# Optimization experiments

Measured on AMD Instinct MI355X. Metric: run time of the kernel, lower is better.

The kernel has to match this reference:

```python
import jax, jax.numpy as jnp
import numpy as np

NEIGHBOR_NUM = 4
POOLING_RATE = 4


def setup_inputs() -> dict:
    key = jax.random.key(0)
    k1, k2, k3 = jax.random.split(key, 3)
    B, N, C = 4, 8192, 256
    vertices = jax.random.normal(k1, (B, N, 3), dtype=jnp.float32)
    feature_map = jax.random.normal(k2, (B, N, C), dtype=jnp.float32)
    pool_num = N // POOLING_RATE
    sample_idx = jax.random.permutation(k3, N)[:pool_num].astype(jnp.int32)  # torch.randperm(N)[:pool_num]
    return {"vertices": vertices, "feature_map": feature_map, "radius": 1, "sample_idx": sample_idx}


def _query_ball_point(radius, nsample, xyz):
    # xyz: [B, N, 3]; self-query (new_xyz == xyz)
    B, N, _ = xyz.shape
    sq = jnp.sum(xyz * xyz, axis=-1)                       # [B, N]
    dist = -2.0 * jnp.einsum('bnc,bmc->bnm', xyz, xyz)     # [B, N, N]
    dist = dist + sq[:, :, None] + sq[:, None, :]
    # original code zeroes the diagonal (self-distance)
    diag = jnp.arange(N)
    dist = dist.at[:, diag, diag].set(0.0)
    # mark out-of-ball entries with sentinel N, sort indices, keep first nsample
    idx = jnp.arange(N, dtype=jnp.int32)
    group_idx = jnp.where(dist > radius ** 2, jnp.int32(N), idx[None, None, :])  # [B, N, N]
    group_idx = jnp.sort(group_idx, axis=-1)[:, :, :nsample]                     # [B, N, nsample]
    group_first = group_idx[:, :, :1]
    group_idx = jnp.where(group_idx == N, group_first, group_idx)
    return group_idx


def reference(vertices, feature_map, radius, sample_idx):
    B, N, _ = vertices.shape
    neighbor_index = _query_ball_point(radius, NEIGHBOR_NUM, vertices)          # [B, N, k]
    bidx = jnp.arange(B)[:, None, None]
    neighbor_feature = feature_map[bidx, neighbor_index]                        # [B, N, k, C]
    pooled_feature = jnp.max(neighbor_feature, axis=2)                          # [B, N, C]
    vertices_pool = vertices[:, sample_idx, :]                                  # [B, pool, 3]
    feature_map_pool = pooled_feature[:, sample_idx, :]                         # [B, pool, C]
    return (vertices_pool, feature_map_pool)
```

## Files before the change

kernel.cpp:

```cpp
#include <hip/hip_runtime.h>


#define BB 4
#define NN 8192
#define CC 256
#define PP 2048
#define KK 4
#define CH 16
#define BATCH (64 * CH)
#define NBATCH (NN / BATCH)

__global__ __launch_bounds__(256) void pool_layer_kernel(
    const float* __restrict__ vertices,
    const float* __restrict__ feat,
    const int*   __restrict__ radius_p,
    const int*   __restrict__ sample_idx,
    float* __restrict__ out_v,
    float* __restrict__ out_f)
{
    const int wave = threadIdx.x >> 6;
    const int lane = threadIdx.x & 63;
    const int q    = blockIdx.x * 4 + wave;
    const int b    = q >> 11;
    const int i    = q & (PP - 1);
    const float* vb = vertices + (size_t)b * NN * 3;

    float px[CH], py[CH], pz[CH];
    #pragma unroll
    for (int c = 0; c < CH; ++c) {
        const int m = c * 64 + lane;
        px[c] = vb[m * 3 + 0];
        py[c] = vb[m * 3 + 1];
        pz[c] = vb[m * 3 + 2];
    }

    const int n = sample_idx[i];
    const float xn0 = vb[n * 3 + 0];
    const float xn1 = vb[n * 3 + 1];
    const float xn2 = vb[n * 3 + 2];
    const float sqn = __fadd_rn(__fadd_rn(__fmul_rn(xn0, xn0),
                                          __fmul_rn(xn1, xn1)),
                                __fmul_rn(xn2, xn2));
    const int   r  = radius_p[0];
    const float r2 = (float)(r * r);

    if (lane < 3) {
        out_v[((size_t)b * PP + i) * 3 + lane] = vb[n * 3 + lane];
    }

    int cand[KK];
    int cnt = 0;
    for (int bat = 0; bat < NBATCH && cnt < KK; ++bat) {
        const int nb = (bat + 1 < NBATCH) ? (bat + 1) : bat;
        float nx[CH], ny[CH], nz[CH];
        #pragma unroll
        for (int c = 0; c < CH; ++c) {
            const int m = nb * BATCH + c * 64 + lane;
            nx[c] = vb[m * 3 + 0];
            ny[c] = vb[m * 3 + 1];
            nz[c] = vb[m * 3 + 2];
        }

        const int base = bat * BATCH;
        unsigned long long masks[CH];
        #pragma unroll
        for (int c = 0; c < CH; ++c) {
            const int m = base + c * 64 + lane;
            const float x0 = px[c], x1 = py[c], x2 = pz[c];
            const float sqm = __fadd_rn(__fadd_rn(__fmul_rn(x0, x0),
                                                  __fmul_rn(x1, x1)),
                                        __fmul_rn(x2, x2));
            const float dot = __fadd_rn(__fadd_rn(__fmul_rn(xn0, x0),
                                                  __fmul_rn(xn1, x1)),
                                        __fmul_rn(xn2, x2));
            const float dist = __fadd_rn(__fadd_rn(__fmul_rn(-2.0f, dot), sqn), sqm);
            masks[c] = __ballot((m == n) || !(dist > r2));
        }
        #pragma unroll
        for (int c = 0; c < CH; ++c) {
            unsigned long long mask = masks[c];
            while (mask && cnt < KK) {
                const int l = __ffsll(mask) - 1;
                cand[cnt++] = base + c * 64 + l;
                mask &= (mask - 1);
            }
        }

        #pragma unroll
        for (int c = 0; c < CH; ++c) { px[c] = nx[c]; py[c] = ny[c]; pz[c] = nz[c]; }
    }
    for (int j = cnt; j < KK; ++j) cand[j] = cand[0];

    const float4* f0 = (const float4*)(feat + ((size_t)b * NN + cand[0]) * CC);
    const float4* f1 = (const float4*)(feat + ((size_t)b * NN + cand[1]) * CC);
    const float4* f2 = (const float4*)(feat + ((size_t)b * NN + cand[2]) * CC);
    const float4* f3 = (const float4*)(feat + ((size_t)b * NN + cand[3]) * CC);
    const float4 a0 = f0[lane];
    const float4 a1 = f1[lane];
    const float4 a2 = f2[lane];
    const float4 a3 = f3[lane];
    float4 o;
    o.x = fmaxf(fmaxf(a0.x, a1.x), fmaxf(a2.x, a3.x));
    o.y = fmaxf(fmaxf(a0.y, a1.y), fmaxf(a2.y, a3.y));
    o.z = fmaxf(fmaxf(a0.z, a1.z), fmaxf(a2.z, a3.z));
    o.w = fmaxf(fmaxf(a0.w, a1.w), fmaxf(a2.w, a3.w));
    ((float4*)(out_f + ((size_t)b * PP + i) * CC))[lane] = o;
}

extern "C" void kernel_launch(void* const* d_in, const int* in_sizes, int n_in,
                              void* d_out, int out_size, void* d_ws, size_t ws_size,
                              hipStream_t stream) {
    const float* vertices   = (const float*)d_in[0];
    const float* feat       = (const float*)d_in[1];
    const int*   radius_p   = (const int*)d_in[2];
    const int*   sample_idx = (const int*)d_in[3];

    float* out_v = (float*)d_out;
    float* out_f = out_v + (size_t)BB * PP * 3;

    const int queries = BB * PP;
    dim3 grid(queries / 4), block(256);
    pool_layer_kernel<<<grid, block, 0, stream>>>(
        vertices, feat, radius_p, sample_idx, out_v, out_f);
}
```

Baseline: 99.39 us.

## Split ball query into fast first-chunk pass and block-parallel straggler kernel

The query kernel now scans only the first 1024 points per query and completes the gather when four neighbours are found. Queries with fewer hits are appended to a worklist via atomics. A second kernel processes them with a full 256-thread block scanning all points and merging the four smallest indices through shared memory. This removes long serial tails from outlier queries, at the cost of an extra memset, a second launch and workspace use.

```diff
diff --git a/kernel.cpp b/kernel.cpp
--- a/kernel.cpp
+++ b/kernel.cpp
@@ -7,22 +7,43 @@
 #define PP 2048
 #define KK 4
 #define CH 16
-#define BATCH (64 * CH)
-#define NBATCH (NN / BATCH)
+#define WS_IDS 64
+#define B_GRID 256
 
-__global__ __launch_bounds__(256) void pool_layer_kernel(
-    const float* __restrict__ vertices,
-    const float* __restrict__ feat,
-    const int*   __restrict__ radius_p,
-    const int*   __restrict__ sample_idx,
-    float* __restrict__ out_v,
-    float* __restrict__ out_f)
-{
+__device__ __forceinline__ float dist_ref(float xn0, float xn1, float xn2, float sqn,
+                                          float x0, float x1, float x2) {
+    const float sqm = __fadd_rn(__fadd_rn(__fmul_rn(x0, x0), __fmul_rn(x1, x1)),
+                                __fmul_rn(x2, x2));
+    const float dot = __fadd_rn(__fadd_rn(__fmul_rn(xn0, x0), __fmul_rn(xn1, x1)),
+                                __fmul_rn(xn2, x2));
+    return __fadd_rn(__fadd_rn(__fmul_rn(-2.0f, dot), sqn), sqm);
+}
+
+__device__ __forceinline__ void gather_maxpool(const float* __restrict__ feat,
+                                               int b, int i, int c0, int c1, int c2, int c3,
+                                               int lane, float* __restrict__ out_f) {
+    const float4 a0 = ((const float4*)(feat + ((size_t)b * NN + c0) * CC))[lane];
+    const float4 a1 = ((const float4*)(feat + ((size_t)b * NN + c1) * CC))[lane];
+    const float4 a2 = ((const float4*)(feat + ((size_t)b * NN + c2) * CC))[lane];
+    const float4 a3 = ((const float4*)(feat + ((size_t)b * NN + c3) * CC))[lane];
+    float4 o;
+    o.x = fmaxf(fmaxf(a0.x, a1.x), fmaxf(a2.x, a3.x));
+    o.y = fmaxf(fmaxf(a0.y, a1.y), fmaxf(a2.y, a3.y));
+    o.z = fmaxf(fmaxf(a0.z, a1.z), fmaxf(a2.z, a3.z));
+    o.w = fmaxf(fmaxf(a0.w, a1.w), fmaxf(a2.w, a3.w));
+    ((float4*)(out_f + ((size_t)b * PP + i) * CC))[lane] = o;
+}
+
+__global__ __launch_bounds__(256) void pool_query_kernel(
+    const float* __restrict__ vertices, const float* __restrict__ feat,
+    const int* __restrict__ radius_p, const int* __restrict__ sample_idx,
+    float* __restrict__ out_v, float* __restrict__ out_f,
+    int* __restrict__ worklist) {
     const int wave = threadIdx.x >> 6;
     const int lane = threadIdx.x & 63;
-    const int q    = blockIdx.x * 4 + wave;
-    const int b    = q >> 11;
-    const int i    = q & (PP - 1);
+    const int q = blockIdx.x * 4 + wave;
+    const int b = q >> 11;
+    const int i = q & (PP - 1);
     const float* vb = vertices + (size_t)b * NN * 3;
 
     float px[CH], py[CH], pz[CH];
@@ -38,73 +59,112 @@
     const float xn0 = vb[n * 3 + 0];
     const float xn1 = vb[n * 3 + 1];
     const float xn2 = vb[n * 3 + 2];
-    const float sqn = __fadd_rn(__fadd_rn(__fmul_rn(xn0, xn0),
-                                          __fmul_rn(xn1, xn1)),
+    const float sqn = __fadd_rn(__fadd_rn(__fmul_rn(xn0, xn0), __fmul_rn(xn1, xn1)),
                                 __fmul_rn(xn2, xn2));
-    const int   r  = radius_p[0];
+    const int r = radius_p[0];
     const float r2 = (float)(r * r);
 
-    if (lane < 3) {
-        out_v[((size_t)b * PP + i) * 3 + lane] = vb[n * 3 + lane];
+    if (lane < 3) out_v[((size_t)b * PP + i) * 3 + lane] = vb[n * 3 + lane];
+
+    int c0 = 0, c1 = 0, c2 = 0, c3 = 0, cnt = 0;
+    #pragma unroll
+    for (int c = 0; c < CH; ++c) {
+        const int m = c * 64 + lane;
+        const float dist = dist_ref(xn0, xn1, xn2, sqn, px[c], py[c], pz[c]);
+        unsigned long long mask = __ballot((m == n) || !(dist > r2));
+        while (mask && cnt < KK) {
+            const int v = c * 64 + (__ffsll((unsigned long long)mask) - 1);
+            c3 = (cnt == 3) ? v : c3;
+            c2 = (cnt == 2) ? v : c2;
+            c1 = (cnt == 1) ? v : c1;
+            c0 = (cnt == 0) ? v : c0;
+            ++cnt;
+            mask &= (mask - 1);
+        }
     }
 
-    int cand[KK];
-    int cnt = 0;
-    for (int bat = 0; bat < NBATCH && cnt < KK; ++bat) {
-        const int nb = (bat + 1 < NBATCH) ? (bat + 1) : bat;
-        float nx[CH], ny[CH], nz[CH];
+    if (cnt >= KK) {
+        gather_maxpool(feat, b, i, c0, c1, c2, c3, lane, out_f);
+    } else if (lane == 0) {
+        const int pos = atomicAdd(worklist, 1);
+        worklist[WS_IDS + pos] = q;
+    }
+}
+
+__global__ __launch_bounds__(256) void pool_straggler_kernel(
+    const float* __restrict__ vertices, const float* __restrict__ feat,
+    const int* __restrict__ radius_p, const int* __restrict__ sample_idx,
+    float* __restrict__ out_f, const int* __restrict__ worklist) {
+    __shared__ int s_loc[256 * 4];
+    __shared__ int s_g[4];
+
+    const int count = worklist[0];
+    const int tid = threadIdx.x;
+    const int lane = tid & 63;
+
+    for (int w = blockIdx.x; w < count; w += gridDim.x) {
+        const int q = worklist[WS_IDS + w];
+        const int b = q >> 11;
+        const int i = q & (PP - 1);
+        const float* vb = vertices + (size_t)b * NN * 3;
+        const int n = sample_idx[i];
+        const float xn0 = vb[n * 3 + 0];
+        const float xn1 = vb[n * 3 + 1];
+        const float xn2 = vb[n * 3 + 2];
+        const float sqn = __fadd_rn(__fadd_rn(__fmul_rn(xn0, xn0), __fmul_rn(xn1, xn1)),
+                                    __fmul_rn(xn2, xn2));
+        const int r = radius_p[0];
+        const float r2 = (float)(r * r);
+
+        int l0 = NN, l1 = NN, l2 = NN, l3 = NN, lcnt = 0;
         #pragma unroll
-        for (int c = 0; c < CH; ++c) {
-            const int m = nb * BATCH + c * 64 + lane;
-            nx[c] = vb[m * 3 + 0];
-            ny[c] = vb[m * 3 + 1];
-            nz[c] = vb[m * 3 + 2];
-        }
-
-        const int base = bat * BATCH;
-        unsigned long long masks[CH];
-        #pragma unroll
-        for (int c = 0; c < CH; ++c) {
-            const int m = base + c * 64 + lane;
-            const float x0 = px[c], x1 = py[c], x2 = pz[c];
-            const float sqm = __fadd_rn(__fadd_rn(__fmul_rn(x0, x0),
-                                                  __fmul_rn(x1, x1)),
-                                        __fmul_rn(x2, x2));
-            const float dot = __fadd_rn(__fadd_rn(__fmul_rn(xn0, x0),
-                                                  __fmul_rn(xn1, x1)),
-                                        __fmul_rn(xn2, x2));
-            const float dist = __fadd_rn(__fadd_rn(__fmul_rn(-2.0f, dot), sqn), sqm);
-            masks[c] = __ballot((m == n) || !(dist > r2));
-        }
-        #pragma unroll
-        for (int c = 0; c < CH; ++c) {
-            unsigned long long mask = masks[c];
-            while (mask && cnt < KK) {
-                const int l = __ffsll(mask) - 1;
-                cand[cnt++] = base + c * 64 + l;
-                mask &= (mask - 1);
+        for (int k = 0; k < NN / 256; ++k) {
+            const int m = k * 256 + tid;
+            const float dist = dist_ref(xn0, xn1, xn2, sqn,
+                                        vb[m * 3 + 0], vb[m * 3 + 1], vb[m * 3 + 2]);
+            const bool hit = (m == n) || !(dist > r2);
+            if (hit) {
+                l3 = (lcnt == 3) ? m : l3;
+                l2 = (lcnt == 2) ? m : l2;
+                l1 = (lcnt == 1) ? m : l1;
+                l0 = (lcnt == 0) ? m : l0;
+                ++lcnt;
             }
         }
+        s_loc[tid * 4 + 0] = l0;
+        s_loc[tid * 4 + 1] = l1;
+        s_loc[tid * 4 + 2] = l2;
+        s_loc[tid * 4 + 3] = l3;
+        __syncthreads();
 
-        #pragma unroll
-        for (int c = 0; c < CH; ++c) { px[c] = nx[c]; py[c] = ny[c]; pz[c] = nz[c]; }
+        if (tid < 64) {
+            int e[16];
+            #pragma unroll
+            for (int j = 0; j < 16; ++j) e[j] = s_loc[tid * 16 + j];
+            int g0, g1, g2, g3;
+            #pragma unroll
+            for (int round = 0; round < 4; ++round) {
+                int m = NN;
+                #pragma unroll
+                for (int j = 0; j < 16; ++j) m = min(m, e[j]);
+                #pragma unroll
+                for (int off = 32; off > 0; off >>= 1)
+                    m = min(m, __shfl_xor(m, off));
+                if (round == 0) g0 = m;
+                if (round == 1) g1 = m;
+                if (round == 2) g2 = m;
+                if (round == 3) g3 = m;
+                #pragma unroll
+                for (int j = 0; j < 16; ++j) e[j] = (e[j] == m) ? NN : e[j];
+            }
+            g1 = (g1 == NN) ? g0 : g1;
+            g2 = (g2 == NN) ? g0 : g2;
+            g3 = (g3 == NN) ? g0 : g3;
+            gather_maxpool(feat, b, i, g0, g1, g2, g3, lane, out_f);
+        }
+        __syncthreads();
     }
-    for (int j = cnt; j < KK; ++j) cand[j] = cand[0];
-
-    const float4* f0 = (const float4*)(feat + ((size_t)b * NN + cand[0]) * CC);
-    const float4* f1 = (const float4*)(feat + ((size_t)b * NN + cand[1]) * CC);
-    const float4* f2 = (const float4*)(feat + ((size_t)b * NN + cand[2]) * CC);
-    const float4* f3 = (const float4*)(feat + ((size_t)b * NN + cand[3]) * CC);
-    const float4 a0 = f0[lane];
-    const float4 a1 = f1[lane];
-    const float4 a2 = f2[lane];
-    const float4 a3 = f3[lane];
-    float4 o;
-    o.x = fmaxf(fmaxf(a0.x, a1.x), fmaxf(a2.x, a3.x));
-    o.y = fmaxf(fmaxf(a0.y, a1.y), fmaxf(a2.y, a3.y));
-    o.z = fmaxf(fmaxf(a0.z, a1.z), fmaxf(a2.z, a3.z));
-    o.w = fmaxf(fmaxf(a0.w, a1.w), fmaxf(a2.w, a3.w));
-    ((float4*)(out_f + ((size_t)b * PP + i) * CC))[lane] = o;
+    (void)s_g;
 }
 
 extern "C" void kernel_launch(void* const* d_in, const int* in_sizes, int n_in,
@@ -117,9 +177,12 @@
 
     float* out_v = (float*)d_out;
     float* out_f = out_v + (size_t)BB * PP * 3;
+    int*   wl    = (int*)d_ws;
 
-    const int queries = BB * PP;
-    dim3 grid(queries / 4), block(256);
-    pool_layer_kernel<<<grid, block, 0, stream>>>(
-        vertices, feat, radius_p, sample_idx, out_v, out_f);
+    hipMemsetAsync(wl, 0, sizeof(int), stream);
+
+    pool_query_kernel<<<dim3(BB * PP / 4), dim3(256), 0, stream>>>(
+        vertices, feat, radius_p, sample_idx, out_v, out_f, wl);
+    pool_straggler_kernel<<<dim3(B_GRID), dim3(256), 0, stream>>>(
+        vertices, feat, radius_p, sample_idx, out_f, wl);
 }
```

Measured after the change: 102.5 us. 1.03x slower.

## Split neighbor search into short first pass and full per-lane fallback scan

Applied to the files above, without the earlier changes.

Replaces the batched prefetch loop with a first pass over only the first 512 points, which usually finds enough in-ball neighbors with random unit-normal data and radius 1. If fewer than four are found, a fallback scans all points with each lane keeping its own first four hits, then merges across the wave with shuffle-min reductions instead of serial ballot extraction. Candidates are kept in scalar registers rather than a dynamically indexed array. The full fallback scan no longer exits early, so queries that need it pay for all points.

```diff
diff --git a/kernel.cpp b/kernel.cpp
--- a/kernel.cpp
+++ b/kernel.cpp
@@ -6,9 +6,18 @@
 #define CC 256
 #define PP 2048
 #define KK 4
-#define CH 16
-#define BATCH (64 * CH)
-#define NBATCH (NN / BATCH)
+#define CH1 8
+#define CH2 16
+#define R2ROUNDS (NN / (64 * CH2))
+
+__device__ __forceinline__ float dist_ref(float xn0, float xn1, float xn2, float sqn,
+                                          float x0, float x1, float x2) {
+    const float sqm = __fadd_rn(__fadd_rn(__fmul_rn(x0, x0), __fmul_rn(x1, x1)),
+                                __fmul_rn(x2, x2));
+    const float dot = __fadd_rn(__fadd_rn(__fmul_rn(xn0, x0), __fmul_rn(xn1, x1)),
+                                __fmul_rn(xn2, x2));
+    return __fadd_rn(__fadd_rn(__fmul_rn(-2.0f, dot), sqn), sqm);
+}
 
 __global__ __launch_bounds__(256) void pool_layer_kernel(
     const float* __restrict__ vertices,
@@ -25,9 +34,9 @@
     const int i    = q & (PP - 1);
     const float* vb = vertices + (size_t)b * NN * 3;
 
-    float px[CH], py[CH], pz[CH];
+    float px[CH1], py[CH1], pz[CH1];
     #pragma unroll
-    for (int c = 0; c < CH; ++c) {
+    for (int c = 0; c < CH1; ++c) {
         const int m = c * 64 + lane;
         px[c] = vb[m * 3 + 0];
         py[c] = vb[m * 3 + 1];
@@ -38,67 +47,75 @@
     const float xn0 = vb[n * 3 + 0];
     const float xn1 = vb[n * 3 + 1];
     const float xn2 = vb[n * 3 + 2];
-    const float sqn = __fadd_rn(__fadd_rn(__fmul_rn(xn0, xn0),
-                                          __fmul_rn(xn1, xn1)),
+    const float sqn = __fadd_rn(__fadd_rn(__fmul_rn(xn0, xn0), __fmul_rn(xn1, xn1)),
                                 __fmul_rn(xn2, xn2));
     const int   r  = radius_p[0];
     const float r2 = (float)(r * r);
 
-    if (lane < 3) {
-        out_v[((size_t)b * PP + i) * 3 + lane] = vb[n * 3 + lane];
+    if (lane < 3) out_v[((size_t)b * PP + i) * 3 + lane] = vb[n * 3 + lane];
+
+    int c0 = 0, c1 = 0, c2 = 0, c3 = 0, cnt = 0;
+    #pragma unroll
+    for (int c = 0; c < CH1; ++c) {
+        const int m = c * 64 + lane;
+        const float dist = dist_ref(xn0, xn1, xn2, sqn, px[c], py[c], pz[c]);
+        unsigned long long mask = __ballot((m == n) || !(dist > r2));
+        while (mask && cnt < KK) {
+            const int v = c * 64 + (__ffsll(mask) - 1);
+            c3 = (cnt == 3) ? v : c3;
+            c2 = (cnt == 2) ? v : c2;
+            c1 = (cnt == 1) ? v : c1;
+            c0 = (cnt == 0) ? v : c0;
+            ++cnt;
+            mask &= (mask - 1);
+        }
     }
 
-    int cand[KK];
-    int cnt = 0;
-    for (int bat = 0; bat < NBATCH && cnt < KK; ++bat) {
-        const int nb = (bat + 1 < NBATCH) ? (bat + 1) : bat;
-        float nx[CH], ny[CH], nz[CH];
-        #pragma unroll
-        for (int c = 0; c < CH; ++c) {
-            const int m = nb * BATCH + c * 64 + lane;
-            nx[c] = vb[m * 3 + 0];
-            ny[c] = vb[m * 3 + 1];
-            nz[c] = vb[m * 3 + 2];
-        }
-
-        const int base = bat * BATCH;
-        unsigned long long masks[CH];
-        #pragma unroll
-        for (int c = 0; c < CH; ++c) {
-            const int m = base + c * 64 + lane;
-            const float x0 = px[c], x1 = py[c], x2 = pz[c];
-            const float sqm = __fadd_rn(__fadd_rn(__fmul_rn(x0, x0),
-                                                  __fmul_rn(x1, x1)),
-                                        __fmul_rn(x2, x2));
-            const float dot = __fadd_rn(__fadd_rn(__fmul_rn(xn0, x0),
-                                                  __fmul_rn(xn1, x1)),
-                                        __fmul_rn(xn2, x2));
-            const float dist = __fadd_rn(__fadd_rn(__fmul_rn(-2.0f, dot), sqn), sqm);
-            masks[c] = __ballot((m == n) || !(dist > r2));
-        }
-        #pragma unroll
-        for (int c = 0; c < CH; ++c) {
-            unsigned long long mask = masks[c];
-            while (mask && cnt < KK) {
-                const int l = __ffsll(mask) - 1;
-                cand[cnt++] = base + c * 64 + l;
-                mask &= (mask - 1);
+    if (cnt < KK) {
+        int l0 = NN, l1 = NN, l2 = NN, l3 = NN, lcnt = 0;
+        for (int base = 0; base < NN; base += 64 * CH2) {
+            float qx[CH2], qy[CH2], qz[CH2];
+            #pragma unroll
+            for (int c = 0; c < CH2; ++c) {
+                const int m = base + c * 64 + lane;
+                qx[c] = vb[m * 3 + 0];
+                qy[c] = vb[m * 3 + 1];
+                qz[c] = vb[m * 3 + 2];
+            }
+            #pragma unroll
+            for (int c = 0; c < CH2; ++c) {
+                const int m = base + c * 64 + lane;
+                const float dist = dist_ref(xn0, xn1, xn2, sqn, qx[c], qy[c], qz[c]);
+                const bool hit = (m == n) || !(dist > r2);
+                if (hit && lcnt < KK) {
+                    l3 = (lcnt == 3) ? m : l3;
+                    l2 = (lcnt == 2) ? m : l2;
+                    l1 = (lcnt == 1) ? m : l1;
+                    l0 = (lcnt == 0) ? m : l0;
+                    ++lcnt;
+                }
             }
         }
+        int g[KK];
+        #pragma unroll
+        for (int round = 0; round < KK; ++round) {
+            int mmin = l0;
+            #pragma unroll
+            for (int off = 32; off > 0; off >>= 1)
+                mmin = min(mmin, __shfl_xor(mmin, off));
+            g[round] = mmin;
+            if (l0 == mmin) { l0 = l1; l1 = l2; l2 = l3; l3 = NN; }
+        }
+        c0 = g[0];
+        c1 = (g[1] == NN) ? g[0] : g[1];
+        c2 = (g[2] == NN) ? g[0] : g[2];
+        c3 = (g[3] == NN) ? g[0] : g[3];
+    }
 
-        #pragma unroll
-        for (int c = 0; c < CH; ++c) { px[c] = nx[c]; py[c] = ny[c]; pz[c] = nz[c]; }
-    }
-    for (int j = cnt; j < KK; ++j) cand[j] = cand[0];
-
-    const float4* f0 = (const float4*)(feat + ((size_t)b * NN + cand[0]) * CC);
-    const float4* f1 = (const float4*)(feat + ((size_t)b * NN + cand[1]) * CC);
-    const float4* f2 = (const float4*)(feat + ((size_t)b * NN + cand[2]) * CC);
-    const float4* f3 = (const float4*)(feat + ((size_t)b * NN + cand[3]) * CC);
-    const float4 a0 = f0[lane];
-    const float4 a1 = f1[lane];
-    const float4 a2 = f2[lane];
-    const float4 a3 = f3[lane];
+    const float4 a0 = ((const float4*)(feat + ((size_t)b * NN + c0) * CC))[lane];
+    const float4 a1 = ((const float4*)(feat + ((size_t)b * NN + c1) * CC))[lane];
+    const float4 a2 = ((const float4*)(feat + ((size_t)b * NN + c2) * CC))[lane];
+    const float4 a3 = ((const float4*)(feat + ((size_t)b * NN + c3) * CC))[lane];
     float4 o;
     o.x = fmaxf(fmaxf(a0.x, a1.x), fmaxf(a2.x, a3.x));
     o.y = fmaxf(fmaxf(a0.y, a1.y), fmaxf(a2.y, a3.y));
@@ -118,8 +135,7 @@
     float* out_v = (float*)d_out;
     float* out_f = out_v + (size_t)BB * PP * 3;
 
-    const int queries = BB * PP;
-    dim3 grid(queries / 4), block(256);
+    dim3 grid(BB * PP / 4), block(256);
     pool_layer_kernel<<<grid, block, 0, stream>>>(
         vertices, feat, radius_p, sample_idx, out_v, out_f);
 }
```

Result: faster. 96.93 us (-2.5%).
